# Kernel optimization log

Hardware: AMD Instinct MI355X
Metric: run time of the kernel (lower is better)

Reference implementation:

```python
import jax, jax.numpy as jnp
import numpy as np

N, E = 131072, 64
REL_SIZES = {0: (262144, 1), 1: (524288, 2), 2: (393216, 3)}  # idx_len, arity


def _mish(x):
    return x * jnp.tanh(jax.nn.softplus(x))


def _mlp(x, rw, rb, ow, ob):
    # torch MLP: output(input + mish(residual(input)))
    return (x + _mish(x @ rw + rb)) @ ow + ob


def setup_inputs() -> dict:
    key = jax.random.key(0)
    ks = jax.random.split(key, 16)

    def lin(k, fi, fo):
        k1, k2 = jax.random.split(k)
        lim = 1.0 / np.sqrt(fi)
        w = jax.random.uniform(k1, (fi, fo), jnp.float32, -lim, lim)
        b = jax.random.uniform(k2, (fo,), jnp.float32, -lim, lim)
        return w, b

    inp = {"obj_emb": jax.random.normal(ks[0], (N, E), jnp.float32)}
    for r in range(3):
        L, _ = REL_SIZES[r]
        inp[f"rel{r}_idx"] = jax.random.randint(ks[1 + r], (L,), 0, N, jnp.int64)
    for r in range(3):
        _, a = REL_SIZES[r]
        d = a * E
        w, b = lin(ks[4 + 2 * r], d, d)
        inp[f"r{r}_res_w"], inp[f"r{r}_res_b"] = w, b
        w, b = lin(ks[5 + 2 * r], d, d)
        inp[f"r{r}_out_w"], inp[f"r{r}_out_b"] = w, b
    w, b = lin(ks[10], 2 * E, 2 * E)
    inp["upd_res_w"], inp["upd_res_b"] = w, b
    w, b = lin(ks[11], 2 * E, E)
    inp["upd_out_w"], inp["upd_out_b"] = w, b
    return inp


def _forward(obj_emb, idxs, rel_params, upd_params):
    n, e = obj_emb.shape
    outs = []
    for (idx, a), (rw, rb, ow, ob) in zip(idxs, rel_params):
        g = obj_emb[idx].reshape(-1, a * e)          # gather -> [T, a*E]
        outs.append((idx, _mlp(g, rw, rb, ow, ob).reshape(-1, e)))
    # First scatter_reduce_('amax', include_self=False): positions written by
    # relation 0 ignore the initial 0; all other positions keep/compete with 0.
    written0 = jnp.zeros((n,), bool).at[idxs[0][0]].set(True)
    m = jnp.broadcast_to(jnp.where(written0[:, None], -jnp.inf, 0.0).astype(obj_emb.dtype), (n, e))
    for idx, out in outs:
        m = m.at[idx].max(out)
    m = jax.lax.stop_gradient(m)
    s = jnp.full((n, e), 1e-16, obj_emb.dtype)
    for idx, out in outs:
        s = s.at[idx].add(jnp.exp(12.0 * (out - m[idx])))
    max_msg = jnp.log(s) / 12.0 + m
    return _mlp(jnp.concatenate([max_msg, obj_emb], axis=1), *upd_params)


def reference(obj_emb, rel0_idx, rel1_idx, rel2_idx,
              r0_res_w, r0_res_b, r0_out_w, r0_out_b,
              r1_res_w, r1_res_b, r1_out_w, r1_out_b,
              r2_res_w, r2_res_b, r2_out_w, r2_out_b,
              upd_res_w, upd_res_b, upd_out_w, upd_out_b):
    idxs = [(rel0_idx, 1), (rel1_idx, 2), (rel2_idx, 3)]
    rel_params = [
        (r0_res_w, r0_res_b, r0_out_w, r0_out_b),
        (r1_res_w, r1_res_b, r1_out_w, r1_out_b),
        (r2_res_w, r2_res_b, r2_out_w, r2_out_b),
    ]
    return _forward(obj_emb, idxs, rel_params,
                    (upd_res_w, upd_res_b, upd_out_w, upd_out_b))
```

## Files before the change

kernel.cpp:

```cpp
#include <hip/hip_runtime.h>
#include <stdint.h>

typedef unsigned short u16;
typedef __bf16 bf16x8 __attribute__((ext_vector_type(8)));
typedef float floatx4 __attribute__((ext_vector_type(4)));

#define N_OBJ    131072
#define L0R      262144
#define L1R      524288
#define L2R      393216
#define TOTI     (L0R + L1R + L2R)


__device__ __forceinline__ float bf2f(u16 u) {
  union { uint32_t i; float f; } v; v.i = ((uint32_t)u) << 16; return v.f;
}
__device__ __forceinline__ u16 f2bf(float f) {
  union { float f; uint32_t i; } v; v.f = f;
  uint32_t r = (v.i + 0x7FFFu + ((v.i >> 16) & 1u)) >> 16;
  return (u16)r;
}
__device__ __forceinline__ u16 f2bf_t(float f) {
  return (u16)(__float_as_uint(f) >> 16);
}
__device__ __forceinline__ uint4 pack8(const float* sp) {
  float4 f0 = *(const float4*)(sp);
  float4 f1 = *(const float4*)(sp + 4);
  uint4 v;
  v.x = (uint32_t)f2bf(f0.x) | ((uint32_t)f2bf(f0.y) << 16);
  v.y = (uint32_t)f2bf(f0.z) | ((uint32_t)f2bf(f0.w) << 16);
  v.z = (uint32_t)f2bf(f1.x) | ((uint32_t)f2bf(f1.y) << 16);
  v.w = (uint32_t)f2bf(f1.z) | ((uint32_t)f2bf(f1.w) << 16);
  return v;
}
__device__ __forceinline__ float mish_f(float x) {
  float t = __expf(fminf(x, 30.f));
  float u = 1.f + t; u = u * u;
  return x * (u - 1.f) * __builtin_amdgcn_rcpf(u + 1.f);
}
#define C12 17.312340490667560f

__global__ __launch_bounds__(256) void pre_kernel(
    const float* __restrict__ emb, u16* __restrict__ ebf,
    const int* __restrict__ r0, const int* __restrict__ r1,
    const int* __restrict__ r2, int* __restrict__ nidx,
    int* __restrict__ cnt, unsigned char* __restrict__ flag,
    const float* w0, const float* w1, const float* w2, const float* w3,
    const float* w4, const float* w5, const float* w6, const float* w7,
    u16* __restrict__ wt, int use_ebf)
{
  int b = blockIdx.x;
  if (b < 4096) {
    if (!use_ebf) return;
    size_t g = (size_t)b * 256 + threadIdx.x;
    *(uint4*)(ebf + g * 8) = pack8(emb + g * 8);
  } else if (b < 4096 + TOTI / 256) {
    int g = (b - 4096) * 256 + (int)threadIdx.x;
    const int* src; int off;
    if (g < L0R)            { src = r0; off = g; }
    else if (g < L0R + L1R) { src = r1; off = g - L0R; }
    else                    { src = r2; off = g - L0R - L1R; }
    int lane = (int)threadIdx.x & 63;
    int probe = src[2 * lane + 1];
    bool i64 = (__ballot(probe == 0) == ~0ull);
    int v = i64 ? src[2 * off] : src[off];
    nidx[g] = v;
    if (g < L0R) flag[v] = 1;
    atomicAdd(&cnt[v], 1);
  } else {
    int bb = b - 4096 - TOTI / 256;
    const float* srcs[8] = {w0, w1, w2, w3, w4, w5, w6, w7};
    const int fi[8]   = {64, 64, 128, 128, 192, 192, 128, 128};
    const int fo[8]   = {64, 64, 128, 128, 192, 192, 128, 64};
    const int boff[9] = {0, 16, 32, 96, 160, 304, 448, 512, 544};
    const int woff[8] = {0, 4096, 8192, 24576, 40960, 77824, 114688, 131072};
    int m = 0;
    #pragma unroll
    for (int j = 0; j < 8; ++j) if (bb >= boff[j + 1]) m = j + 1;
    int e = (bb - boff[m]) * 256 + (int)threadIdx.x;
    int k = e / fo[m];
    int n = e - k * fo[m];
    wt[woff[m] + n * fi[m] + k] = f2bf(srcs[m][e]);
  }
}

__global__ __launch_bounds__(256) void scan_a(
    const int* __restrict__ count, int* __restrict__ thrpre,
    int* __restrict__ blocksum)
{
  int tid = (int)threadIdx.x, b = blockIdx.x;
  int o = b * 1024 + tid * 4;
  int t = count[o] + count[o + 1] + count[o + 2] + count[o + 3];
  __shared__ int sd[256];
  sd[tid] = t; __syncthreads();
  for (int off = 1; off < 256; off <<= 1) {
    int v = (tid >= off) ? sd[tid - off] : 0;
    __syncthreads();
    sd[tid] += v;
    __syncthreads();
  }
  thrpre[b * 256 + tid] = sd[tid] - t;
  if (tid == 255) blocksum[b] = sd[tid];
}
__global__ __launch_bounds__(128) void scan_b(int* __restrict__ blocksum)
{
  int tid = (int)threadIdx.x;
  int t = blocksum[tid];
  __shared__ int sd[128];
  sd[tid] = t; __syncthreads();
  for (int off = 1; off < 128; off <<= 1) {
    int v = (tid >= off) ? sd[tid - off] : 0;
    __syncthreads();
    sd[tid] += v;
    __syncthreads();
  }
  blocksum[tid] = sd[tid] - t;
}
__global__ __launch_bounds__(256) void scan_c(
    const int* __restrict__ count, const int* __restrict__ thrpre,
    const int* __restrict__ blocksum, int* __restrict__ offsets,
    int* __restrict__ cursor)
{
  int tid = (int)threadIdx.x, b = blockIdx.x;
  int o = b * 1024 + tid * 4;
  int base = blocksum[b] + thrpre[b * 256 + tid];
  #pragma unroll
  for (int j = 0; j < 4; ++j) {
    offsets[o + j] = base;
    cursor[o + j] = base;
    base += count[o + j];
  }
}

template<int D, int DOUT, int ROWS, int EBF>
__device__ __forceinline__ void mlp_body(
    char* smem, const float* __restrict__ srcF, const u16* __restrict__ srcB,
    const int* __restrict__ idx, int bidx,
    const u16* __restrict__ rwt, const float* __restrict__ rb,
    const u16* __restrict__ owt, const float* __restrict__ ob,
    u16* __restrict__ msg, int* __restrict__ cursor)
{
  constexpr int A = D / 64;
  constexpr int PITCH = D + 8;
  constexpr int KI = D / 32;
  constexpr int CT1 = D / 64;
  constexpr int CT2 = DOUT / 64;
  constexpr int RT = ROWS / 16;
  u16*   g_lds  = (u16*)smem;
  float* b1_lds = (float*)(smem + ROWS * PITCH * 2);
  float* b2_lds = b1_lds + D;
  int*   i_lds  = (int*)(b2_lds + DOUT);
  int*   p_lds  = i_lds + ROWS * A;

  const int tid = threadIdx.x;
  const int wave = tid >> 6;
  const int lane = tid & 63;
  const int q = lane >> 4;
  const int i = lane & 15;
  const int t0 = bidx * ROWS;

  for (int c = tid; c < D; c += 256) b1_lds[c] = rb[c];
  for (int c = tid; c < DOUT; c += 256) b2_lds[c] = ob[c] * C12;
  for (int c = tid; c < ROWS * A; c += 256) {
    int obj = idx[t0 * A + c];
    i_lds[c] = obj;
    p_lds[c] = atomicAdd(&cursor[obj], 1);
  }

  for (int c = tid; c < ROWS * A * 8; c += 256) {
    int e = c >> 3, p = c & 7;
    int r = e / A, sl = e - r * A;
    int obj = idx[(t0 + r) * A + sl];
    uint4 val = EBF ? *(const uint4*)(srcB + (size_t)obj * 64 + p * 8)
                    : pack8(srcF + (size_t)obj * 64 + p * 8);
    *(uint4*)(&g_lds[r * PITCH + sl * 64 + p * 8]) = val;
  }
  __syncthreads();

  bf16x8 af[KI];

  bf16x8 b1[CT1][KI];
  #pragma unroll
  for (int j = 0; j < CT1; ++j)
    #pragma unroll
    for (int k = 0; k < KI; ++k)
      b1[j][k] = *(const bf16x8*)(rwt +
          (size_t)((wave * CT1 + j) * 16 + i) * D + k * 32 + q * 8);

  floatx4 acc1[RT][CT1];
  #pragma unroll
  for (int rt = 0; rt < RT; ++rt)
    #pragma unroll
    for (int j = 0; j < CT1; ++j) acc1[rt][j] = (floatx4)0.f;

  #pragma unroll
  for (int rt = 0; rt < RT; ++rt) {
    #pragma unroll
    for (int k = 0; k < KI; ++k)
      af[k] = *(const bf16x8*)(&g_lds[(rt * 16 + i) * PITCH + k * 32 + q * 8]);
    #pragma unroll
    for (int j = 0; j < CT1; ++j)
      #pragma unroll
      for (int k = 0; k < KI; ++k)
        acc1[rt][j] = __builtin_amdgcn_mfma_f32_16x16x32_bf16(
            af[k], b1[j][k], acc1[rt][j], 0, 0, 0);
  }
  __syncthreads();

  #pragma unroll
  for (int rt = 0; rt < RT; ++rt)
    #pragma unroll
    for (int j = 0; j < CT1; ++j) {
      int col = (wave * CT1 + j) * 16 + i;
      #pragma unroll
      for (int r = 0; r < 4; ++r) {
        int row = rt * 16 + q * 4 + r;
        float h = acc1[rt][j][r] + b1_lds[col];
        float g = bf2f(g_lds[row * PITCH + col]);
        g_lds[row * PITCH + col] = f2bf_t(g + mish_f(h));
      }
    }
  __syncthreads();

  bf16x8 b2[CT2][KI];
  #pragma unroll
  for (int j = 0; j < CT2; ++j)
    #pragma unroll
    for (int k = 0; k < KI; ++k)
      b2[j][k] = *(const bf16x8*)(owt +
          (size_t)((wave * CT2 + j) * 16 + i) * D + k * 32 + q * 8);

  floatx4 acc2[RT][CT2];
  #pragma unroll
  for (int rt = 0; rt < RT; ++rt)
    #pragma unroll
    for (int j = 0; j < CT2; ++j) acc2[rt][j] = (floatx4)0.f;

  #pragma unroll
  for (int rt = 0; rt < RT; ++rt) {
    #pragma unroll
    for (int k = 0; k < KI; ++k)
      af[k] = *(const bf16x8*)(&g_lds[(rt * 16 + i) * PITCH + k * 32 + q * 8]);
    #pragma unroll
    for (int j = 0; j < CT2; ++j)
      #pragma unroll
      for (int k = 0; k < KI; ++k)
        acc2[rt][j] = __builtin_amdgcn_mfma_f32_16x16x32_bf16(
            af[k], b2[j][k], acc2[rt][j], 0, 0, 0);
  }
  __syncthreads();

  #pragma unroll
  for (int rt = 0; rt < RT; ++rt)
    #pragma unroll
    for (int j = 0; j < CT2; ++j) {
      int col = (wave * CT2 + j) * 16 + i;
      #pragma unroll
      for (int r = 0; r < 4; ++r) {
        int row = rt * 16 + q * 4 + r;
        float z = fminf(fmaf(acc2[rt][j][r], C12, b2_lds[col]), 118.f);
        g_lds[row * PITCH + col] = f2bf_t(exp2f(z));
      }
    }
  __syncthreads();
  for (int c = tid; c < ROWS * A * 8; c += 256) {
    int e = c >> 3, p = c & 7;
    int r = e / A, sl = e - r * A;
    int pos = p_lds[r * A + sl];
    *(uint4*)(msg + (size_t)pos * 64 + p * 8) =
        *(const uint4*)(&g_lds[r * PITCH + sl * 64 + p * 8]);
  }
}

template<int EBF>
__global__ __launch_bounds__(256, 3) void rel_merged(
    const float* __restrict__ srcF, const u16* __restrict__ ebf,
    const int* __restrict__ nidx, const u16* __restrict__ wt,
    const float* __restrict__ r0rb, const float* __restrict__ r0ob,
    const float* __restrict__ r1rb, const float* __restrict__ r1ob,
    const float* __restrict__ r2rb, const float* __restrict__ r2ob,
    u16* __restrict__ msg, int* __restrict__ cursor)
{
  extern __shared__ char smem[];
  int b = blockIdx.x;
  int g3 = b / 3, m = b - g3 * 3;
  if (m == 0)
    mlp_body<64, 64, 64, EBF>(smem, srcF, ebf, nidx, g3,
                              wt + 0, r0rb, wt + 4096, r0ob, msg, cursor);
  else if (m == 1)
    mlp_body<128, 128, 64, EBF>(smem, srcF, ebf, nidx + L0R, g3,
                                wt + 8192, r1rb, wt + 24576, r1ob, msg, cursor);
  else
    mlp_body<192, 192, 32, EBF>(smem, srcF, ebf, nidx + L0R + L1R, g3,
                                wt + 40960, r2rb, wt + 77824, r2ob, msg, cursor);
}

template<int EBF>
__global__ __launch_bounds__(256, 4) void upd_fused(
    const float* __restrict__ srcF, const u16* __restrict__ ebf,
    const u16* __restrict__ msg, const int* __restrict__ count,
    const int* __restrict__ offsets, const unsigned char* __restrict__ flag,
    const u16* __restrict__ rwt, const float* __restrict__ rb,
    const u16* __restrict__ owt, const float* __restrict__ ob,
    float* __restrict__ dstF)
{
  constexpr int D = 128, DOUT = 64;
  constexpr int PITCH = D + 8;
  constexpr int KI = D / 32;
  constexpr int CT1 = 2, CT2 = 1;
  __shared__ alignas(16) u16 g_lds[64 * PITCH];
  __shared__ float b1_lds[D];
  __shared__ float b2_lds[DOUT];

  const int tid = threadIdx.x;
  const int wave = tid >> 6;
  const int lane = tid & 63;
  const int q = lane >> 4;
  const int i = lane & 15;
  const int t0 = blockIdx.x * 64;

  for (int c = tid; c < D; c += 256) b1_lds[c] = rb[c];
  for (int c = tid; c < DOUT; c += 256) b2_lds[c] = ob[c];

  for (int c = tid; c < 64 * 2 * 8; c += 256) {
    int e = c >> 3, p = c & 7;
    int r = e >> 1, sl = e & 1;
    int o = t0 + r;
    if (sl == 0) {
      int deg = count[o], st = offsets[o];
      const u16* bp = msg + (size_t)st * 64 + p * 8;
      float s[8] = {0.f, 0.f, 0.f, 0.f, 0.f, 0.f, 0.f, 0.f};
      for (int j = 0; j < deg; ++j) {
        union { uint4 v; u16 a[8]; } ld;
        ld.v = *(const uint4*)(bp + (size_t)j * 64);
        #pragma unroll
        for (int k = 0; k < 8; ++k) s[k] += bf2f(ld.a[k]);
      }
      float add = flag[o] ? 1e-37f : 1e-16f;
      u16 tmp[8];
      #pragma unroll
      for (int k = 0; k < 8; ++k)
        tmp[k] = f2bf(__logf(s[k] + add) * (1.f / 12.f));
      *(uint4*)(&g_lds[r * PITCH + p * 8]) = *(uint4*)tmp;
    } else {
      uint4 val = EBF ? *(const uint4*)(ebf + (size_t)o * 64 + p * 8)
                      : pack8(srcF + (size_t)o * 64 + p * 8);
      *(uint4*)(&g_lds[r * PITCH + 64 + p * 8]) = val;
    }
  }
  __syncthreads();

  bf16x8 af[KI];
  bf16x8 b1[CT1][KI];
  #pragma unroll
  for (int j = 0; j < CT1; ++j)
    #pragma unroll
    for (int k = 0; k < KI; ++k)
      b1[j][k] = *(const bf16x8*)(rwt +
          (size_t)((wave * CT1 + j) * 16 + i) * D + k * 32 + q * 8);

  floatx4 acc1[4][CT1];
  #pragma unroll
  for (int rt = 0; rt < 4; ++rt)
    #pragma unroll
    for (int j = 0; j < CT1; ++j) acc1[rt][j] = (floatx4)0.f;

  #pragma unroll
  for (int rt = 0; rt < 4; ++rt) {
    #pragma unroll
    for (int k = 0; k < KI; ++k)
      af[k] = *(const bf16x8*)(&g_lds[(rt * 16 + i) * PITCH + k * 32 + q * 8]);
    #pragma unroll
    for (int j = 0; j < CT1; ++j)
      #pragma unroll
      for (int k = 0; k < KI; ++k)
        acc1[rt][j] = __builtin_amdgcn_mfma_f32_16x16x32_bf16(
            af[k], b1[j][k], acc1[rt][j], 0, 0, 0);
  }
  __syncthreads();

  #pragma unroll
  for (int rt = 0; rt < 4; ++rt)
    #pragma unroll
    for (int j = 0; j < CT1; ++j) {
      int col = (wave * CT1 + j) * 16 + i;
      #pragma unroll
      for (int r = 0; r < 4; ++r) {
        int row = rt * 16 + q * 4 + r;
        float h = acc1[rt][j][r] + b1_lds[col];
        float g = bf2f(g_lds[row * PITCH + col]);
        g_lds[row * PITCH + col] = f2bf_t(g + mish_f(h));
      }
    }
  __syncthreads();

  bf16x8 b2[CT2][KI];
  #pragma unroll
  for (int j = 0; j < CT2; ++j)
    #pragma unroll
    for (int k = 0; k < KI; ++k)
      b2[j][k] = *(const bf16x8*)(owt +
          (size_t)((wave * CT2 + j) * 16 + i) * D + k * 32 + q * 8);

  floatx4 acc2[4][CT2];
  #pragma unroll
  for (int rt = 0; rt < 4; ++rt)
    #pragma unroll
    for (int j = 0; j < CT2; ++j) acc2[rt][j] = (floatx4)0.f;

  #pragma unroll
  for (int rt = 0; rt < 4; ++rt) {
    #pragma unroll
    for (int k = 0; k < KI; ++k)
      af[k] = *(const bf16x8*)(&g_lds[(rt * 16 + i) * PITCH + k * 32 + q * 8]);
    #pragma unroll
    for (int j = 0; j < CT2; ++j)
      #pragma unroll
      for (int k = 0; k < KI; ++k)
        acc2[rt][j] = __builtin_amdgcn_mfma_f32_16x16x32_bf16(
            af[k], b2[j][k], acc2[rt][j], 0, 0, 0);
  }

  #pragma unroll
  for (int rt = 0; rt < 4; ++rt) {
    int col = wave * 16 + i;
    #pragma unroll
    for (int r = 0; r < 4; ++r) {
      int row = rt * 16 + q * 4 + r;
      dstF[(size_t)(t0 + row) * 64 + col] = acc2[rt][0][r] + b2_lds[col];
    }
  }
}

template<int D, int DOUT, int MODE>
__global__ __launch_bounds__(256, (D >= 192) ? 3 : 4) void mlp_fb(
    const float* __restrict__ srcF, const u16* __restrict__ srcM,
    const int* __restrict__ idx,
    const u16* __restrict__ rwt, const float* __restrict__ rb,
    const u16* __restrict__ owt, const float* __restrict__ ob,
    float* __restrict__ dstF, float* __restrict__ sAt)
{
  constexpr int A = D / 64;
  constexpr int PITCH = D + 8;
  constexpr int KI = D / 32;
  constexpr int CT1 = D / 64;
  constexpr int CT2 = DOUT / 64;
  __shared__ alignas(16) u16 g_lds[64 * PITCH];
  __shared__ float b1_lds[D];
  __shared__ float b2_lds[DOUT];
  __shared__ int i_lds[64 * A];

  const int tid = threadIdx.x;
  const int wave = tid >> 6;
  const int lane = tid & 63;
  const int q = lane >> 4;
  const int i = lane & 15;
  const int t0 = blockIdx.x * 64;

  for (int c = tid; c < D; c += 256) b1_lds[c] = rb[c];
  for (int c = tid; c < DOUT; c += 256) b2_lds[c] = ob[c];
  if (MODE != 1)
    for (int c = tid; c < 64 * A; c += 256) i_lds[c] = idx[t0 * A + c];

  for (int c = tid; c < 64 * A * 8; c += 256) {
    int e = c >> 3, p = c & 7;
    int r = e / A, sl = e - r * A;
    uint4 val;
    if (MODE != 1) {
      int obj = idx[(t0 + r) * A + sl];
      val = pack8(srcF + (size_t)obj * 64 + p * 8);
    } else {
      if (sl == 0) val = *(const uint4*)(srcM + (size_t)(t0 + r) * 64 + p * 8);
      else         val = pack8(srcF + (size_t)(t0 + r) * 64 + p * 8);
    }
    *(uint4*)(&g_lds[r * PITCH + sl * 64 + p * 8]) = val;
  }
  __syncthreads();

  bf16x8 af[KI];
  bf16x8 b1[CT1][KI];
  #pragma unroll
  for (int j = 0; j < CT1; ++j)
    #pragma unroll
    for (int k = 0; k < KI; ++k)
      b1[j][k] = *(const bf16x8*)(rwt +
          (size_t)((wave * CT1 + j) * 16 + i) * D + k * 32 + q * 8);
  floatx4 acc1[4][CT1];
  #pragma unroll
  for (int rt = 0; rt < 4; ++rt)
    #pragma unroll
    for (int j = 0; j < CT1; ++j) acc1[rt][j] = (floatx4)0.f;
  #pragma unroll
  for (int rt = 0; rt < 4; ++rt) {
    #pragma unroll
    for (int k = 0; k < KI; ++k)
      af[k] = *(const bf16x8*)(&g_lds[(rt * 16 + i) * PITCH + k * 32 + q * 8]);
    #pragma unroll
    for (int j = 0; j < CT1; ++j)
      #pragma unroll
      for (int k = 0; k < KI; ++k)
        acc1[rt][j] = __builtin_amdgcn_mfma_f32_16x16x32_bf16(
            af[k], b1[j][k], acc1[rt][j], 0, 0, 0);
  }
  __syncthreads();
  #pragma unroll
  for (int rt = 0; rt < 4; ++rt)
    #pragma unroll
    for (int j = 0; j < CT1; ++j) {
      int col = (wave * CT1 + j) * 16 + i;
      #pragma unroll
      for (int r = 0; r < 4; ++r) {
        int row = rt * 16 + q * 4 + r;
        float h = acc1[rt][j][r] + b1_lds[col];
        float g = bf2f(g_lds[row * PITCH + col]);
        g_lds[row * PITCH + col] = f2bf(g + mish_f(h));
      }
    }
  __syncthreads();
  bf16x8 b2[CT2][KI];
  #pragma unroll
  for (int j = 0; j < CT2; ++j)
    #pragma unroll
    for (int k = 0; k < KI; ++k)
      b2[j][k] = *(const bf16x8*)(owt +
          (size_t)((wave * CT2 + j) * 16 + i) * D + k * 32 + q * 8);
  floatx4 acc2[4][CT2];
  #pragma unroll
  for (int rt = 0; rt < 4; ++rt)
    #pragma unroll
    for (int j = 0; j < CT2; ++j) acc2[rt][j] = (floatx4)0.f;
  #pragma unroll
  for (int rt = 0; rt < 4; ++rt) {
    #pragma unroll
    for (int k = 0; k < KI; ++k)
      af[k] = *(const bf16x8*)(&g_lds[(rt * 16 + i) * PITCH + k * 32 + q * 8]);
    #pragma unroll
    for (int j = 0; j < CT2; ++j)
      #pragma unroll
      for (int k = 0; k < KI; ++k)
        acc2[rt][j] = __builtin_amdgcn_mfma_f32_16x16x32_bf16(
            af[k], b2[j][k], acc2[rt][j], 0, 0, 0);
  }
  #pragma unroll
  for (int rt = 0; rt < 4; ++rt)
    #pragma unroll
    for (int j = 0; j < CT2; ++j) {
      int col = (wave * CT2 + j) * 16 + i;
      #pragma unroll
      for (int r = 0; r < 4; ++r) {
        int row = rt * 16 + q * 4 + r;
        float y = acc2[rt][j][r] + b2_lds[col];
        if (MODE == 2) {
          int slot = col >> 6, cc = col & 63;
          int obj = i_lds[row * A + slot];
          atomicAdd(&sAt[(size_t)obj * 64 + cc], __expf(fminf(12.f * y, 82.f)));
        } else {
          dstF[(size_t)(t0 + row) * 64 + col] = y;
        }
      }
    }
}

__global__ __launch_bounds__(256) void norm_fb(
    const int* __restrict__ r0, const int* __restrict__ r1,
    const int* __restrict__ r2, int* __restrict__ n,
    unsigned char* __restrict__ flag)
{
  int g = blockIdx.x * 256 + (int)threadIdx.x;
  const int* src; int off;
  if (g < L0R)            { src = r0; off = g; }
  else if (g < L0R + L1R) { src = r1; off = g - L0R; }
  else                    { src = r2; off = g - L0R - L1R; }
  int lane = (int)threadIdx.x & 63;
  int probe = src[2 * lane + 1];
  bool i64 = (__ballot(probe == 0) == ~0ull);
  int v = i64 ? src[2 * off] : src[off];
  n[g] = v;
  if (g < L0R) flag[v] = 1;
}

__global__ __launch_bounds__(256) void prep_fb(
    const float* w0, const float* w1, const float* w2, const float* w3,
    const float* w4, const float* w5, const float* w6, const float* w7,
    u16* __restrict__ wt)
{
  int b = blockIdx.x;
  const float* srcs[8] = {w0, w1, w2, w3, w4, w5, w6, w7};
  const int fi[8]   = {64, 64, 128, 128, 192, 192, 128, 128};
  const int fo[8]   = {64, 64, 128, 128, 192, 192, 128, 64};
  const int boff[9] = {0, 16, 32, 96, 160, 304, 448, 512, 544};
  const int woff[8] = {0, 4096, 8192, 24576, 40960, 77824, 114688, 131072};
  int m = 0;
  #pragma unroll
  for (int j = 0; j < 8; ++j) if (b >= boff[j + 1]) m = j + 1;
  int e = (b - boff[m]) * 256 + (int)threadIdx.x;
  int k = e / fo[m];
  int n = e - k * fo[m];
  wt[woff[m] + n * fi[m] + k] = f2bf(srcs[m][e]);
}

__global__ __launch_bounds__(256) void final_kernel(
    const float* __restrict__ s, const unsigned char* __restrict__ flag,
    u16* __restrict__ maxmsg)
{
  int tid = (int)threadIdx.x;
  int o = blockIdx.x * 64 + (tid >> 2);
  int c0 = (tid & 3) * 16;
  float add = flag[o] ? 1e-37f : 1e-16f;
  const float* sp = s + (size_t)o * 64 + c0;
  u16* mp = maxmsg + (size_t)o * 64 + c0;
  u16 tmp[16];
  #pragma unroll
  for (int j = 0; j < 16; ++j)
    tmp[j] = f2bf(__logf(sp[j] + add) * (1.f / 12.f));
  *(uint4*)(mp)     = *(uint4*)(tmp);
  *(uint4*)(mp + 8) = *(uint4*)(tmp + 8);
}

extern "C" void kernel_launch(void* const* d_in, const int* in_sizes, int n_in,
                              void* d_out, int out_size, void* d_ws, size_t ws_size,
                              hipStream_t stream)
{
  (void)in_sizes; (void)n_in; (void)out_size;
  const float* obj_emb = (const float*)d_in[0];
  const float* r0rb = (const float*)d_in[5];
  const float* r0ob = (const float*)d_in[7];
  const float* r1rb = (const float*)d_in[9];
  const float* r1ob = (const float*)d_in[11];
  const float* r2rb = (const float*)d_in[13];
  const float* r2ob = (const float*)d_in[15];
  const float* urb  = (const float*)d_in[17];
  const float* uob  = (const float*)d_in[19];
  float* out = (float*)d_out;
  char* ws = (char*)d_ws;

  const size_t NEED1 = 174605312ull;
  const size_t NEED2 = NEED1 + 16777216ull;

  if (ws_size >= NEED1) {
    u16* msg           = (u16*)(ws);
    u16* wt            = (u16*)(ws + 150994944ull);
    unsigned char* flg = (unsigned char*)(ws + 151273472ull);
    int* nidx          = (int*)(ws + 168181760ull);
    int* count         = (int*)(ws + 172900352ull);
    int* offsets       = (int*)(ws + 173424640ull);
    int* cursor        = (int*)(ws + 173948928ull);
    int* thrpre        = (int*)(ws + 174473216ull);
    int* blocksum      = (int*)(ws + 174604288ull);
    u16* ebf           = (u16*)(ws + 174605312ull);
    int use_ebf = (ws_size >= NEED2) ? 1 : 0;

    hipMemsetAsync(count, 0, N_OBJ * 4, stream);
    hipMemsetAsync(flg, 0, N_OBJ, stream);

    pre_kernel<<<4096 + TOTI / 256 + 544, 256, 0, stream>>>(
        obj_emb, ebf,
        (const int*)d_in[1], (const int*)d_in[2], (const int*)d_in[3],
        nidx, count, flg,
        (const float*)d_in[4], (const float*)d_in[6], (const float*)d_in[8],
        (const float*)d_in[10], (const float*)d_in[12], (const float*)d_in[14],
        (const float*)d_in[16], (const float*)d_in[18], wt, use_ebf);
    scan_a<<<128, 256, 0, stream>>>(count, thrpre, blocksum);
    scan_b<<<1, 128, 0, stream>>>(blocksum);
    scan_c<<<128, 256, 0, stream>>>(count, thrpre, blocksum, offsets, cursor);

    if (use_ebf) {
      rel_merged<1><<<12288, 256, 19456, stream>>>(
          obj_emb, ebf, nidx, wt, r0rb, r0ob, r1rb, r1ob, r2rb, r2ob, msg, cursor);
      upd_fused<1><<<2048, 256, 0, stream>>>(
          obj_emb, ebf, msg, count, offsets, flg,
          wt + 114688, urb, wt + 131072, uob, out);
    } else {
      rel_merged<0><<<12288, 256, 19456, stream>>>(
          obj_emb, ebf, nidx, wt, r0rb, r0ob, r1rb, r1ob, r2rb, r2ob, msg, cursor);
      upd_fused<0><<<2048, 256, 0, stream>>>(
          obj_emb, ebf, msg, count, offsets, flg,
          wt + 114688, urb, wt + 131072, uob, out);
    }
  } else {
    float* s           = (float*)(ws);
    u16* wt            = (u16*)(ws + 33554432ull);
    unsigned char* flg = (unsigned char*)(ws + 33832960ull);
    u16* maxmsg        = (u16*)(ws + 33964032ull);
    int* nidx          = (int*)(ws + 50741248ull);

    hipMemsetAsync(s, 0, 64ull * N_OBJ * 4ull, stream);
    hipMemsetAsync(flg, 0, N_OBJ, stream);

    norm_fb<<<TOTI / 256, 256, 0, stream>>>(
        (const int*)d_in[1], (const int*)d_in[2], (const int*)d_in[3], nidx, flg);
    prep_fb<<<544, 256, 0, stream>>>(
        (const float*)d_in[4], (const float*)d_in[6], (const float*)d_in[8],
        (const float*)d_in[10], (const float*)d_in[12], (const float*)d_in[14],
        (const float*)d_in[16], (const float*)d_in[18], wt);

    mlp_fb<64, 64, 2><<<4096, 256, 0, stream>>>(
        obj_emb, nullptr, nidx, wt + 0, r0rb, wt + 4096, r0ob, nullptr, s);
    mlp_fb<128, 128, 2><<<4096, 256, 0, stream>>>(
        obj_emb, nullptr, nidx + L0R, wt + 8192, r1rb, wt + 24576, r1ob, nullptr, s);
    mlp_fb<192, 192, 2><<<2048, 256, 0, stream>>>(
        obj_emb, nullptr, nidx + L0R + L1R, wt + 40960, r2rb, wt + 77824, r2ob,
        nullptr, s);

    final_kernel<<<N_OBJ / 64, 256, 0, stream>>>(s, flg, maxmsg);

    mlp_fb<128, 64, 1><<<2048, 256, 0, stream>>>(
        obj_emb, maxmsg, nullptr, wt + 114688, urb, wt + 131072, uob, out, nullptr);
  }
}
```

Baseline: 401.3 us.

## Make relation MLP blocks persistent with register-prefetched gather of next tile

Each relation block now processes four row tiles in a strided loop instead of one. The gather and cursor atomics for the next tile are issued into registers while the current tile's two MFMA GEMMs run, and p_lds is double-buffered. Relation 2 moves from 32 to 64 rows per tile, the grid shrinks from 12288 to 2560 blocks, and shared memory grows. The aim is to hide gather latency and cut per-block launch overhead, at the cost of more registers (greg), fewer blocks to balance load, and possibly lower occupancy.

```diff
diff --git a/kernel.cpp b/kernel.cpp
--- a/kernel.cpp
+++ b/kernel.cpp
@@ -132,10 +132,10 @@
   }
 }
 
-template<int D, int DOUT, int ROWS, int EBF>
+template<int D, int DOUT, int ROWS, int T, int EBF>
 __device__ __forceinline__ void mlp_body(
     char* smem, const float* __restrict__ srcF, const u16* __restrict__ srcB,
-    const int* __restrict__ idx, int bidx,
+    const int* __restrict__ idx, int bi, int tstride,
     const u16* __restrict__ rwt, const float* __restrict__ rb,
     const u16* __restrict__ owt, const float* __restrict__ ob,
     u16* __restrict__ msg, int* __restrict__ cursor)
@@ -146,129 +146,146 @@
   constexpr int CT1 = D / 64;
   constexpr int CT2 = DOUT / 64;
   constexpr int RT = ROWS / 16;
+  constexpr int RA = ROWS * A;
+  constexpr int NG = RA * 8 / 256;
   u16*   g_lds  = (u16*)smem;
   float* b1_lds = (float*)(smem + ROWS * PITCH * 2);
   float* b2_lds = b1_lds + D;
-  int*   i_lds  = (int*)(b2_lds + DOUT);
-  int*   p_lds  = i_lds + ROWS * A;
+  int*   p_lds  = (int*)(b2_lds + DOUT);
 
   const int tid = threadIdx.x;
   const int wave = tid >> 6;
   const int lane = tid & 63;
   const int q = lane >> 4;
   const int i = lane & 15;
-  const int t0 = bidx * ROWS;
 
   for (int c = tid; c < D; c += 256) b1_lds[c] = rb[c];
   for (int c = tid; c < DOUT; c += 256) b2_lds[c] = ob[c] * C12;
-  for (int c = tid; c < ROWS * A; c += 256) {
-    int obj = idx[t0 * A + c];
-    i_lds[c] = obj;
-    p_lds[c] = atomicAdd(&cursor[obj], 1);
-  }
-
-  for (int c = tid; c < ROWS * A * 8; c += 256) {
-    int e = c >> 3, p = c & 7;
-    int r = e / A, sl = e - r * A;
-    int obj = idx[(t0 + r) * A + sl];
-    uint4 val = EBF ? *(const uint4*)(srcB + (size_t)obj * 64 + p * 8)
+
+  uint4 greg[NG];
+
+  auto prefetch = [&](int tt) {
+    const int* ib = idx + (size_t)(bi + tt * tstride) * RA;
+    for (int c = tid; c < RA; c += 256)
+      p_lds[(tt & 1) * RA + c] = atomicAdd(&cursor[ib[c]], 1);
+    #pragma unroll
+    for (int u = 0; u < NG; ++u) {
+      int c = u * 256 + tid;
+      int e = c >> 3, p = c & 7;
+      int r = e / A, sl = e - r * A;
+      int obj = ib[r * A + sl];
+      greg[u] = EBF ? *(const uint4*)(srcB + (size_t)obj * 64 + p * 8)
                     : pack8(srcF + (size_t)obj * 64 + p * 8);
-    *(uint4*)(&g_lds[r * PITCH + sl * 64 + p * 8]) = val;
-  }
-  __syncthreads();
-
-  bf16x8 af[KI];
-
-  bf16x8 b1[CT1][KI];
-  #pragma unroll
-  for (int j = 0; j < CT1; ++j)
-    #pragma unroll
-    for (int k = 0; k < KI; ++k)
-      b1[j][k] = *(const bf16x8*)(rwt +
-          (size_t)((wave * CT1 + j) * 16 + i) * D + k * 32 + q * 8);
-
-  floatx4 acc1[RT][CT1];
-  #pragma unroll
-  for (int rt = 0; rt < RT; ++rt)
-    #pragma unroll
-    for (int j = 0; j < CT1; ++j) acc1[rt][j] = (floatx4)0.f;
-
-  #pragma unroll
-  for (int rt = 0; rt < RT; ++rt) {
-    #pragma unroll
-    for (int k = 0; k < KI; ++k)
-      af[k] = *(const bf16x8*)(&g_lds[(rt * 16 + i) * PITCH + k * 32 + q * 8]);
+    }
+  };
+
+  prefetch(0);
+
+  for (int tt = 0; tt < T; ++tt) {
+    __syncthreads();
+    #pragma unroll
+    for (int u = 0; u < NG; ++u) {
+      int c = u * 256 + tid;
+      int e = c >> 3, p = c & 7;
+      int r = e / A, sl = e - r * A;
+      *(uint4*)(&g_lds[r * PITCH + sl * 64 + p * 8]) = greg[u];
+    }
+    __syncthreads();
+    if (tt + 1 < T) prefetch(tt + 1);
+
+    bf16x8 af[KI];
+
+    bf16x8 b1[CT1][KI];
     #pragma unroll
     for (int j = 0; j < CT1; ++j)
       #pragma unroll
       for (int k = 0; k < KI; ++k)
-        acc1[rt][j] = __builtin_amdgcn_mfma_f32_16x16x32_bf16(
-            af[k], b1[j][k], acc1[rt][j], 0, 0, 0);
-  }
-  __syncthreads();
-
-  #pragma unroll
-  for (int rt = 0; rt < RT; ++rt)
-    #pragma unroll
-    for (int j = 0; j < CT1; ++j) {
-      int col = (wave * CT1 + j) * 16 + i;
-      #pragma unroll
-      for (int r = 0; r < 4; ++r) {
-        int row = rt * 16 + q * 4 + r;
-        float h = acc1[rt][j][r] + b1_lds[col];
-        float g = bf2f(g_lds[row * PITCH + col]);
-        g_lds[row * PITCH + col] = f2bf_t(g + mish_f(h));
+        b1[j][k] = *(const bf16x8*)(rwt +
+            (size_t)((wave * CT1 + j) * 16 + i) * D + k * 32 + q * 8);
+
+    floatx4 acc1[RT][CT1];
+    #pragma unroll
+    for (int rt = 0; rt < RT; ++rt)
+      #pragma unroll
+      for (int j = 0; j < CT1; ++j) acc1[rt][j] = (floatx4)0.f;
+
+    #pragma unroll
+    for (int rt = 0; rt < RT; ++rt) {
+      #pragma unroll
+      for (int k = 0; k < KI; ++k)
+        af[k] = *(const bf16x8*)(&g_lds[(rt * 16 + i) * PITCH + k * 32 + q * 8]);
+      #pragma unroll
+      for (int j = 0; j < CT1; ++j)
+        #pragma unroll
+        for (int k = 0; k < KI; ++k)
+          acc1[rt][j] = __builtin_amdgcn_mfma_f32_16x16x32_bf16(
+              af[k], b1[j][k], acc1[rt][j], 0, 0, 0);
+    }
+    __syncthreads();
+
+    #pragma unroll
+    for (int rt = 0; rt < RT; ++rt)
+      #pragma unroll
+      for (int j = 0; j < CT1; ++j) {
+        int col = (wave * CT1 + j) * 16 + i;
+        #pragma unroll
+        for (int r = 0; r < 4; ++r) {
+          int row = rt * 16 + q * 4 + r;
+          float h = acc1[rt][j][r] + b1_lds[col];
+          float g = bf2f(g_lds[row * PITCH + col]);
+          g_lds[row * PITCH + col] = f2bf_t(g + mish_f(h));
+        }
       }
-    }
-  __syncthreads();
-
-  bf16x8 b2[CT2][KI];
-  #pragma unroll
-  for (int j = 0; j < CT2; ++j)
-    #pragma unroll
-    for (int k = 0; k < KI; ++k)
-      b2[j][k] = *(const bf16x8*)(owt +
-          (size_t)((wave * CT2 + j) * 16 + i) * D + k * 32 + q * 8);
-
-  floatx4 acc2[RT][CT2];
-  #pragma unroll
-  for (int rt = 0; rt < RT; ++rt)
-    #pragma unroll
-    for (int j = 0; j < CT2; ++j) acc2[rt][j] = (floatx4)0.f;
-
-  #pragma unroll
-  for (int rt = 0; rt < RT; ++rt) {
-    #pragma unroll
-    for (int k = 0; k < KI; ++k)
-      af[k] = *(const bf16x8*)(&g_lds[(rt * 16 + i) * PITCH + k * 32 + q * 8]);
+    __syncthreads();
+
+    bf16x8 b2[CT2][KI];
     #pragma unroll
     for (int j = 0; j < CT2; ++j)
       #pragma unroll
       for (int k = 0; k < KI; ++k)
-        acc2[rt][j] = __builtin_amdgcn_mfma_f32_16x16x32_bf16(
-            af[k], b2[j][k], acc2[rt][j], 0, 0, 0);
-  }
-  __syncthreads();
-
-  #pragma unroll
-  for (int rt = 0; rt < RT; ++rt)
-    #pragma unroll
-    for (int j = 0; j < CT2; ++j) {
-      int col = (wave * CT2 + j) * 16 + i;
-      #pragma unroll
-      for (int r = 0; r < 4; ++r) {
-        int row = rt * 16 + q * 4 + r;
-        float z = fminf(fmaf(acc2[rt][j][r], C12, b2_lds[col]), 118.f);
-        g_lds[row * PITCH + col] = f2bf_t(exp2f(z));
+        b2[j][k] = *(const bf16x8*)(owt +
+            (size_t)((wave * CT2 + j) * 16 + i) * D + k * 32 + q * 8);
+
+    floatx4 acc2[RT][CT2];
+    #pragma unroll
+    for (int rt = 0; rt < RT; ++rt)
+      #pragma unroll
+      for (int j = 0; j < CT2; ++j) acc2[rt][j] = (floatx4)0.f;
+
+    #pragma unroll
+    for (int rt = 0; rt < RT; ++rt) {
+      #pragma unroll
+      for (int k = 0; k < KI; ++k)
+        af[k] = *(const bf16x8*)(&g_lds[(rt * 16 + i) * PITCH + k * 32 + q * 8]);
+      #pragma unroll
+      for (int j = 0; j < CT2; ++j)
+        #pragma unroll
+        for (int k = 0; k < KI; ++k)
+          acc2[rt][j] = __builtin_amdgcn_mfma_f32_16x16x32_bf16(
+              af[k], b2[j][k], acc2[rt][j], 0, 0, 0);
+    }
+    __syncthreads();
+
+    #pragma unroll
+    for (int rt = 0; rt < RT; ++rt)
+      #pragma unroll
+      for (int j = 0; j < CT2; ++j) {
+        int col = (wave * CT2 + j) * 16 + i;
+        #pragma unroll
+        for (int r = 0; r < 4; ++r) {
+          int row = rt * 16 + q * 4 + r;
+          float z = fminf(fmaf(acc2[rt][j][r], C12, b2_lds[col]), 118.f);
+          g_lds[row * PITCH + col] = f2bf_t(exp2f(z));
+        }
       }
-    }
-  __syncthreads();
-  for (int c = tid; c < ROWS * A * 8; c += 256) {
-    int e = c >> 3, p = c & 7;
-    int r = e / A, sl = e - r * A;
-    int pos = p_lds[r * A + sl];
-    *(uint4*)(msg + (size_t)pos * 64 + p * 8) =
-        *(const uint4*)(&g_lds[r * PITCH + sl * 64 + p * 8]);
+    __syncthreads();
+    for (int c = tid; c < RA * 8; c += 256) {
+      int e = c >> 3, p = c & 7;
+      int r = e / A, sl = e - r * A;
+      int pos = p_lds[(tt & 1) * RA + r * A + sl];
+      *(uint4*)(msg + (size_t)pos * 64 + p * 8) =
+          *(const uint4*)(&g_lds[r * PITCH + sl * 64 + p * 8]);
+    }
   }
 }
 
@@ -283,16 +300,16 @@
 {
   extern __shared__ char smem[];
   int b = blockIdx.x;
-  int g3 = b / 3, m = b - g3 * 3;
-  if (m == 0)
-    mlp_body<64, 64, 64, EBF>(smem, srcF, ebf, nidx, g3,
-                              wt + 0, r0rb, wt + 4096, r0ob, msg, cursor);
-  else if (m == 1)
-    mlp_body<128, 128, 64, EBF>(smem, srcF, ebf, nidx + L0R, g3,
-                                wt + 8192, r1rb, wt + 24576, r1ob, msg, cursor);
+  int g5 = b / 5, m = b - g5 * 5;
+  if (m < 2)
+    mlp_body<64, 64, 64, 4, EBF>(smem, srcF, ebf, nidx, g5 * 2 + m, 1024,
+                                 wt + 0, r0rb, wt + 4096, r0ob, msg, cursor);
+  else if (m < 4)
+    mlp_body<128, 128, 64, 4, EBF>(smem, srcF, ebf, nidx + L0R, g5 * 2 + (m - 2),
+                                   1024, wt + 8192, r1rb, wt + 24576, r1ob, msg, cursor);
   else
-    mlp_body<192, 192, 32, EBF>(smem, srcF, ebf, nidx + L0R + L1R, g3,
-                                wt + 40960, r2rb, wt + 77824, r2ob, msg, cursor);
+    mlp_body<192, 192, 64, 4, EBF>(smem, srcF, ebf, nidx + L0R + L1R, g5, 512,
+                                   wt + 40960, r2rb, wt + 77824, r2ob, msg, cursor);
 }
 
 template<int EBF>
@@ -665,13 +682,13 @@
     scan_c<<<128, 256, 0, stream>>>(count, thrpre, blocksum, offsets, cursor);
 
     if (use_ebf) {
-      rel_merged<1><<<12288, 256, 19456, stream>>>(
+      rel_merged<1><<<2560, 256, 28672, stream>>>(
           obj_emb, ebf, nidx, wt, r0rb, r0ob, r1rb, r1ob, r2rb, r2ob, msg, cursor);
       upd_fused<1><<<2048, 256, 0, stream>>>(
           obj_emb, ebf, msg, count, offsets, flg,
           wt + 114688, urb, wt + 131072, uob, out);
     } else {
-      rel_merged<0><<<12288, 256, 19456, stream>>>(
+      rel_merged<0><<<2560, 256, 28672, stream>>>(
           obj_emb, ebf, nidx, wt, r0rb, r0ob, r1rb, r1ob, r2rb, r2ob, msg, cursor);
       upd_fused<0><<<2048, 256, 0, stream>>>(
           obj_emb, ebf, msg, count, offsets, flg,
```

Result: slower. 447.8 us (+11.6%).
